# Kernel optimization log

Hardware: AMD Instinct MI355X
Metric: run time of the kernel (lower is better)

## Reference

```python
import jax, jax.numpy as jnp
import numpy as np

V, D, NH, DH, DFF, NL = 32000, 512, 8, 64, 2048, 6
S, B = 512, 8
NEG = -1e18


def layer_norm(x, g, b, eps=1e-5):
    m = x.mean(-1, keepdims=True)
    v = ((x - m) ** 2).mean(-1, keepdims=True)
    return (x - m) / jnp.sqrt(v + eps) * g + b


def mha(q, k, v, Wq, bq, Wk, bk, Wv, bv, Wo, bo, mask):
    Bq, Q, _ = q.shape
    K = k.shape[1]
    qh = (q @ Wq + bq).reshape(Bq, Q, NH, DH).transpose(0, 2, 1, 3)
    kh = (k @ Wk + bk).reshape(Bq, K, NH, DH).transpose(0, 2, 1, 3)
    vh = (v @ Wv + bv).reshape(Bq, K, NH, DH).transpose(0, 2, 1, 3)
    scores = jnp.einsum('bhqd,bhkd->bhqk', qh, kh) / np.sqrt(DH).astype(np.float32)
    scores = jnp.where(mask[:, None, :, :], NEG, scores)
    attn = jax.nn.softmax(scores, axis=-1)
    ctx = jnp.einsum('bhqk,bhkd->bhqd', attn, vh).transpose(0, 2, 1, 3).reshape(Bq, Q, NH * DH)
    return ctx @ Wo + bo


def positional_encoding(seq_len):
    pos = jnp.arange(seq_len, dtype=jnp.float32)[:, None]
    div = jnp.exp(jnp.arange(0, D, 2, dtype=jnp.float32) * (-np.log(10000.0) / D))
    pe = jnp.zeros((seq_len, D), jnp.float32)
    pe = pe.at[:, 0::2].set(jnp.sin(pos * div))
    pe = pe.at[:, 1::2].set(jnp.cos(pos * div))
    return pe


def setup_inputs() -> dict:
    key = jax.random.key(0)
    ks = iter(jax.random.split(key, 64))
    sc = 0.02
    pn = lambda shape: jax.random.normal(next(ks), shape, jnp.float32) * sc
    inp = {}
    inp['targets'] = jax.random.randint(next(ks), (S, B), 0, V)
    inp['memory'] = jax.random.normal(next(ks), (B, S, D), jnp.float32)
    inp['trg_mask'] = jnp.broadcast_to(jnp.triu(jnp.ones((S, S), bool), 1), (B, S, S))
    inp['memory_mask'] = jnp.zeros((B, S, S), bool)
    emb = pn((V, D)).at[1].set(0.0)  # padding_idx=1
    inp['emb'] = emb
    # stacked per-layer params
    for nm in ['Wq_s', 'Wk_s', 'Wv_s', 'Wo_s', 'Wq_c', 'Wk_c', 'Wv_c', 'Wo_c']:
        inp[nm] = pn((NL, D, D))
    for nm in ['bq_s', 'bk_s', 'bv_s', 'bo_s', 'bq_c', 'bk_c', 'bv_c', 'bo_c']:
        inp[nm] = jnp.zeros((NL, D), jnp.float32)
    inp['W1'] = pn((NL, D, DFF)); inp['b1'] = jnp.zeros((NL, DFF), jnp.float32)
    inp['W2'] = pn((NL, DFF, D)); inp['b2'] = jnp.zeros((NL, D), jnp.float32)
    for nm in ['g1', 'g2', 'g3']:
        inp[nm] = jnp.ones((NL, D), jnp.float32)
    for nm in ['be1', 'be2', 'be3']:
        inp[nm] = jnp.zeros((NL, D), jnp.float32)
    return inp


def reference(targets, memory, trg_mask, memory_mask, emb,
              Wq_s, bq_s, Wk_s, bk_s, Wv_s, bv_s, Wo_s, bo_s,
              Wq_c, bq_c, Wk_c, bk_c, Wv_c, bv_c, Wo_c, bo_c,
              W1, b1, W2, b2, g1, be1, g2, be2, g3, be3):
    # targets: (S, B) ints; embedding + sqrt(d) scale + sinusoidal PE
    x = emb[targets] * np.sqrt(D).astype(np.float32)      # (S, B, D)
    x = x + positional_encoding(targets.shape[0])[:, None, :]
    x = x.transpose(1, 0, 2)                              # (B, S, D)
    for i in range(NL):
        sa = mha(x, x, x, Wq_s[i], bq_s[i], Wk_s[i], bk_s[i], Wv_s[i], bv_s[i],
                 Wo_s[i], bo_s[i], trg_mask)
        x = layer_norm(x + sa, g1[i], be1[i])
        ca = mha(x, memory, memory, Wq_c[i], bq_c[i], Wk_c[i], bk_c[i], Wv_c[i], bv_c[i],
                 Wo_c[i], bo_c[i], memory_mask)
        x = layer_norm(x + ca, g2[i], be2[i])
        ff = jax.nn.relu(x @ W1[i] + b1[i]) @ W2[i] + b2[i]
        x = layer_norm(x + ff, g3[i], be3[i])
    return x
```

## Files before the change

### kernel.cpp

```cpp
#include <hip/hip_runtime.h>

typedef unsigned short u16;
typedef unsigned int   u32;
typedef __attribute__((ext_vector_type(4))) u16   u16x4;
typedef __attribute__((ext_vector_type(8))) u16   u16x8;
typedef __attribute__((ext_vector_type(8))) __bf16 bf16x8;
typedef __attribute__((ext_vector_type(4))) float f32x4;

#define DEV static __device__ __forceinline__

constexpr int DIM = 512, NHEAD = 8, DHEAD = 64, DFFN = 2048, NLAY = 6, SEQ = 512, BATCH = 8;
constexpr int MROWS = BATCH * SEQ;
constexpr long HD = (long)SEQ * DHEAD;
constexpr long SQ = (long)DIM * DIM;

DEV float bf2f(u16 u) { union { u32 i; float f; } x; x.i = (u32)u << 16; return x.f; }
DEV u16 f2bf(float f) { union { float f; u32 i; } x; x.f = f; u32 r = x.i + 0x7fffu + ((x.i >> 16) & 1u); return (u16)(r >> 16); }

DEV void gl_lds16(const u16* g, u16* l) {
    __builtin_amdgcn_global_load_lds((const __attribute__((address_space(1))) u32*)(const void*)g,
                                     (__attribute__((address_space(3))) u32*)(void*)l, 16, 0, 0);
}

struct TP { const float* in[8]; u16* out[8]; long ls[8]; };

__global__ __launch_bounds__(256) void transpose8(TP p)
{
    __shared__ u16 t[32][33];
    int z = blockIdx.z, which = z / NLAY, l = z % NLAY;
    const float* in = p.in[which] + (long)l * SQ;
    u16* out = p.out[which] + (long)l * p.ls[which];
    int k0 = blockIdx.y * 32, n0 = blockIdx.x * 32;
    int tx = threadIdx.x & 31, ty = threadIdx.x >> 5;
    #pragma unroll
    for (int i = ty; i < 32; i += 8) t[i][tx] = f2bf(in[(long)(k0 + i) * 512 + n0 + tx]);
    __syncthreads();
    #pragma unroll
    for (int i = ty; i < 32; i += 8) out[(long)(n0 + i) * 512 + k0 + tx] = t[tx][i];
}

__global__ __launch_bounds__(256) void transpose_w(const float* __restrict__ in, u16* __restrict__ out,
                                                   int K, int N, long outLS)
{
    __shared__ u16 t[32][33];
    long bi = (long)blockIdx.z * K * N, bo = (long)blockIdx.z * outLS;
    int k0 = blockIdx.y * 32, n0 = blockIdx.x * 32;
    int tx = threadIdx.x & 31, ty = threadIdx.x >> 5;
    #pragma unroll
    for (int i = ty; i < 32; i += 8) t[i][tx] = f2bf(in[bi + (long)(k0 + i) * N + n0 + tx]);
    __syncthreads();
    #pragma unroll
    for (int i = ty; i < 32; i += 8) out[bo + (long)(n0 + i) * K + k0 + tx] = t[tx][i];
}

__global__ __launch_bounds__(256) void concat_bias(const float* __restrict__ a, const float* __restrict__ b,
                                                   const float* __restrict__ c, float* __restrict__ out, int nsrc)
{
    int i = blockIdx.x * 256 + threadIdx.x;
    int col = i & 511, j = (i >> 9) % nsrc, l = i / (nsrc * 512);
    const float* s = (j == 0) ? a : (j == 1) ? b : c;
    out[i] = s[l * 512 + col];
}

__global__ __launch_bounds__(256) void conv_f32_bf16(const float* __restrict__ in, u16* __restrict__ out)
{
    long i = ((long)blockIdx.x * 256 + threadIdx.x) * 4;
    float4 v = *(const float4*)(in + i);
    u16x4 o; o.x = f2bf(v.x); o.y = f2bf(v.y); o.z = f2bf(v.z); o.w = f2bf(v.w);
    *(u16x4*)(out + i) = o;
}

__global__ __launch_bounds__(256) void embed_pe(const int* __restrict__ targets, const float* __restrict__ emb,
                                                float* __restrict__ x, u16* __restrict__ xb)
{
    int t4 = (blockIdx.x * 256 + threadIdx.x) * 4;
    int d = t4 & (DIM - 1);
    int s = (t4 >> 9) & (SEQ - 1);
    int b = t4 >> 18;
    int tok = targets[s * BATCH + b];
    float4 e = *(const float4*)(emb + (long)tok * DIM + d);
    float o[4]; u16x4 ob;
    const float ef[4] = { e.x, e.y, e.z, e.w };
    #pragma unroll
    for (int j = 0; j < 4; ++j) {
        int dd = d + j;
        float div = expf((float)(dd & ~1) * -0.017988946039016f);
        float ang = (float)s * div;
        float pe = (dd & 1) ? cosf(ang) : sinf(ang);
        float val = ef[j] * 22.627416997969522f + pe;
        o[j] = val; ob[j] = f2bf(val);
    }
    long idx = ((long)b * SEQ + s) * DIM + d;
    *(float4*)(x + idx) = *(const float4*)o;
    *(u16x4*)(xb + idx) = ob;
}

DEV void scat_sd(u16* dst, int mm, int col, float v) {
    dst[(long)((mm >> 9) * NHEAD + (col >> 6)) * HD + (long)(mm & 511) * DHEAD + (col & 63)] = f2bf(v);
}
DEV void scat_ds(u16* dst, int mm, int col, float v) {
    dst[(long)((mm >> 9) * NHEAD + (col >> 6)) * HD + (long)(col & 63) * SEQ + (mm & 511)] = f2bf(v);
}

template <int BN, int EPI>
__global__ __launch_bounds__(256) void gemm64(const u16* __restrict__ A0, const u16* __restrict__ A1,
                                              const u16* __restrict__ Bt,
                                              void* __restrict__ C0, void* __restrict__ C1, void* __restrict__ C2,
                                              const float* __restrict__ bias, int K, int ldc, int gx, int aSplit)
{
    constexpr int NCH = (64 + BN) / 8;
    constexpr int NI  = BN / 32;
    __shared__ __align__(16) u16 lds[2][NCH * 512];

    const int tid = threadIdx.x, lane = tid & 63, wid = tid >> 6;
    const int nwg = gridDim.x, bid = blockIdx.x;
    const int wg = (bid & 7) * (nwg >> 3) + (bid >> 3);
    const int m0 = (wg / gx) * 64, n0 = (wg % gx) * BN;
    const u16* A = (n0 < aSplit) ? A0 : A1;
    const int wr = (wid >> 1) * 32, wc = (wid & 1) * (BN / 2);
    const int fr = lane & 15, fq = lane >> 4;
    const int srow = lane >> 3;
    const int scol = ((lane & 7) ^ srow) * 8;

    f32x4 acc[2][NI] = {};

    auto stage = [&](int buf, int k0) {
        #pragma unroll
        for (int c = wid; c < 8; c += 4)
            gl_lds16(A + (long)(m0 + c * 8 + srow) * K + k0 + scol, &lds[buf][c * 512]);
        #pragma unroll
        for (int c = 8 + wid; c < NCH; c += 4)
            gl_lds16(Bt + (long)(n0 + (c - 8) * 8 + srow) * K + k0 + scol, &lds[buf][c * 512]);
    };

    const int nt = K >> 6;
    stage(0, 0);
    __syncthreads();
    int cur = 0;
    const int swz = (fr & 7) << 4;
    for (int t = 0; t < nt; ++t) {
        if (t + 1 < nt) stage(cur ^ 1, (t + 1) << 6);
        const char* lb = (const char*)&lds[cur][0];
        bf16x8 a[2][2], b[NI][2];
        #pragma unroll
        for (int mi = 0; mi < 2; ++mi)
            #pragma unroll
            for (int kk = 0; kk < 2; ++kk)
                a[mi][kk] = *(const bf16x8*)(lb + (wr + mi * 16 + fr) * 128 + ((kk * 64 + fq * 16) ^ swz));
        #pragma unroll
        for (int ni = 0; ni < NI; ++ni)
            #pragma unroll
            for (int kk = 0; kk < 2; ++kk)
                b[ni][kk] = *(const bf16x8*)(lb + (64 + wc + ni * 16 + fr) * 128 + ((kk * 64 + fq * 16) ^ swz));
        #pragma unroll
        for (int kk = 0; kk < 2; ++kk)
            #pragma unroll
            for (int mi = 0; mi < 2; ++mi)
                #pragma unroll
                for (int ni = 0; ni < NI; ++ni)
                    acc[mi][ni] = __builtin_amdgcn_mfma_f32_16x16x32_bf16(a[mi][kk], b[ni][kk], acc[mi][ni], 0, 0, 0);
        __syncthreads();
        cur ^= 1;
    }

    #pragma unroll
    for (int mi = 0; mi < 2; ++mi)
    #pragma unroll
    for (int ni = 0; ni < NI; ++ni)
    #pragma unroll
    for (int rr = 0; rr < 4; ++rr) {
        int mm = m0 + wr + mi * 16 + fq * 4 + rr;
        int nn = n0 + wc + ni * 16 + fr;
        float v = acc[mi][ni][rr] + bias[nn];
        if (EPI == 0) {
            ((u16*)C0)[(long)mm * ldc + nn] = f2bf(v);
        } else if (EPI == 1) {
            ((u16*)C0)[(long)mm * ldc + nn] = f2bf(fmaxf(v, 0.f));
        } else {
            int which = nn >> 9, col = nn & 511;
            if (which == 0)      scat_sd((u16*)C0, mm, col, v);
            else if (which == 1) scat_sd((u16*)C1, mm, col, v);
            else                 scat_ds((u16*)C2, mm, col, v);
        }
    }
}

template <bool CAUSAL>
__global__ __launch_bounds__(256) void flash_attn(const u16* __restrict__ qh, const u16* __restrict__ kh,
                                                  const u16* __restrict__ vT, u16* __restrict__ ctx)
{
    constexpr int KVB = 128;
    __shared__ __align__(16) u16 Kl[2][KVB * 64];
    __shared__ __align__(16) u16 Vl[2][64 * KVB];
    __shared__ __align__(16) u16 Pl[4][16 * KVB];
    const int lane = threadIdx.x & 63, wid = threadIdx.x >> 6;
    const int head = blockIdx.x >> 3, qt = blockIdx.x & 7;
    const int q0 = qt * 64;
    const long hb = (long)head * HD;
    const int fr = lane & 15, fq = lane >> 4;

    bf16x8 qf[2];
    #pragma unroll
    for (int kf = 0; kf < 2; ++kf)
        qf[kf] = *(const bf16x8*)(qh + hb + (long)(q0 + wid * 16 + fr) * 64 + kf * 32 + fq * 8);

    const int nt = CAUSAL ? (q0 >> 7) + 1 : SEQ / KVB;

    auto stage = [&](int buf, int t) {
        const long kv0 = (long)t * KVB;
        for (int c = wid; c < 16; c += 4)
            gl_lds16(kh + hb + (kv0 + c * 8 + (lane >> 3)) * 64 + (lane & 7) * 8, &Kl[buf][c * 512]);
        for (int c = wid; c < 16; c += 4)
            gl_lds16(vT + hb + (long)(c * 4 + (lane >> 4)) * SEQ + kv0 + (lane & 15) * 8, &Vl[buf][c * 512]);
    };

    float m[4], l[4];
    #pragma unroll
    for (int r = 0; r < 4; ++r) { m[r] = -3.0e38f; l[r] = 0.f; }
    f32x4 ao[4] = {};

    stage(0, 0);
    __syncthreads();
    int cur = 0;
    for (int t = 0; t < nt; ++t) {
        if (t + 1 < nt) stage(cur ^ 1, t + 1);
        f32x4 as[8] = {};
        #pragma unroll
        for (int nf = 0; nf < 8; ++nf)
            #pragma unroll
            for (int kf = 0; kf < 2; ++kf) {
                bf16x8 kfr = *(const bf16x8*)&Kl[cur][(nf * 16 + fr) * 64 + kf * 32 + fq * 8];
                as[nf] = __builtin_amdgcn_mfma_f32_16x16x32_bf16(qf[kf], kfr, as[nf], 0, 0, 0);
            }
        const int kv0 = t * KVB;
        const int qrow = q0 + wid * 16 + fq * 4;
        #pragma unroll
        for (int nf = 0; nf < 8; ++nf)
            #pragma unroll
            for (int rr = 0; rr < 4; ++rr) {
                float s = as[nf][rr] * 0.125f;
                if (CAUSAL && (kv0 + nf * 16 + fr > qrow + rr)) s = -3.0e38f;
                as[nf][rr] = s;
            }
        float p_scale[4];
        #pragma unroll
        for (int rr = 0; rr < 4; ++rr) {
            float mx = as[0][rr];
            #pragma unroll
            for (int nf = 1; nf < 8; ++nf) mx = fmaxf(mx, as[nf][rr]);
            #pragma unroll
            for (int o = 1; o < 16; o <<= 1) mx = fmaxf(mx, __shfl_xor(mx, o, 64));
            float mnew = fmaxf(m[rr], mx);
            p_scale[rr] = __expf(m[rr] - mnew);
            m[rr] = mnew;
        }
        float rsum[4] = {0.f, 0.f, 0.f, 0.f};
        u16* pw = &Pl[wid][0];
        #pragma unroll
        for (int nf = 0; nf < 8; ++nf)
            #pragma unroll
            for (int rr = 0; rr < 4; ++rr) {
                float p = __expf(as[nf][rr] - m[rr]);
                rsum[rr] += p;
                int row = fq * 4 + rr;
                int byte = (row * 256 + (nf * 16 + fr) * 2) ^ ((row & 7) << 4);
                *(u16*)((char*)pw + byte) = f2bf(p);
            }
        #pragma unroll
        for (int rr = 0; rr < 4; ++rr) {
            #pragma unroll
            for (int o = 1; o < 16; o <<= 1) rsum[rr] += __shfl_xor(rsum[rr], o, 64);
            l[rr] = l[rr] * p_scale[rr] + rsum[rr];
        }
        #pragma unroll
        for (int nf = 0; nf < 4; ++nf)
            #pragma unroll
            for (int rr = 0; rr < 4; ++rr) ao[nf][rr] *= p_scale[rr];
        #pragma unroll
        for (int kf = 0; kf < 4; ++kf) {
            int byte = (fr * 256 + kf * 64 + fq * 16) ^ ((fr & 7) << 4);
            bf16x8 pa = *(const bf16x8*)((const char*)pw + byte);
            #pragma unroll
            for (int nf = 0; nf < 4; ++nf) {
                bf16x8 vf = *(const bf16x8*)&Vl[cur][(nf * 16 + fr) * KVB + kf * 32 + fq * 8];
                ao[nf] = __builtin_amdgcn_mfma_f32_16x16x32_bf16(pa, vf, ao[nf], 0, 0, 0);
            }
        }
        __syncthreads();
        cur ^= 1;
    }
    const int b = head >> 3, h = head & 7;
    #pragma unroll
    for (int nf = 0; nf < 4; ++nf)
        #pragma unroll
        for (int rr = 0; rr < 4; ++rr) {
            int qq = q0 + wid * 16 + fq * 4 + rr;
            ctx[((long)(b * SEQ + qq)) * DIM + h * 64 + nf * 16 + fr] = f2bf(ao[nf][rr] / l[rr]);
        }
}

__global__ __launch_bounds__(256) void add_ln(const float* x, const u16* __restrict__ y,
                                              float* xo, u16* __restrict__ xb,
                                              const float* __restrict__ g, const float* __restrict__ be)
{
    int row = blockIdx.x * 4 + (threadIdx.x >> 6);
    int lane = threadIdx.x & 63;
    long off = (long)row * DIM + lane * 8;
    float v[8];
    {
        float4 a0 = *(const float4*)(x + off);
        float4 a1 = *(const float4*)(x + off + 4);
        u16x8 yv = *(const u16x8*)(y + off);
        v[0] = a0.x + bf2f(yv[0]); v[1] = a0.y + bf2f(yv[1]);
        v[2] = a0.z + bf2f(yv[2]); v[3] = a0.w + bf2f(yv[3]);
        v[4] = a1.x + bf2f(yv[4]); v[5] = a1.y + bf2f(yv[5]);
        v[6] = a1.z + bf2f(yv[6]); v[7] = a1.w + bf2f(yv[7]);
    }
    float sum = 0.f;
    #pragma unroll
    for (int j = 0; j < 8; ++j) sum += v[j];
    #pragma unroll
    for (int o = 32; o; o >>= 1) sum += __shfl_xor(sum, o, 64);
    float mean = sum * (1.0f / DIM);
    float vs = 0.f;
    #pragma unroll
    for (int j = 0; j < 8; ++j) { float d = v[j] - mean; vs += d * d; }
    #pragma unroll
    for (int o = 32; o; o >>= 1) vs += __shfl_xor(vs, o, 64);
    float rstd = rsqrtf(vs * (1.0f / DIM) + 1e-5f);
    float outv[8]; u16x8 ob;
    #pragma unroll
    for (int j = 0; j < 8; ++j) {
        int col = lane * 8 + j;
        float r = (v[j] - mean) * rstd * g[col] + be[col];
        outv[j] = r; ob[j] = f2bf(r);
    }
    *(float4*)(xo + off)     = *(const float4*)&outv[0];
    *(float4*)(xo + off + 4) = *(const float4*)&outv[4];
    *(u16x8*)(xb + off) = ob;
}

extern "C" void kernel_launch(void* const* d_in, const int* in_sizes, int n_in,
                              void* d_out, int out_size, void* d_ws, size_t ws_size,
                              hipStream_t stream)
{
    const int*   targets = (const int*)  d_in[0];
    const float* memory  = (const float*)d_in[1];
    const float* emb     = (const float*)d_in[4];
    const float* Wg[8]; for (int i = 0; i < 8; ++i) Wg[i] = (const float*)d_in[5 + i];
    const float* bg[8]; for (int i = 0; i < 8; ++i) bg[i] = (const float*)d_in[13 + i];
    const float* W1  = (const float*)d_in[21];
    const float* b1  = (const float*)d_in[22];
    const float* W2  = (const float*)d_in[23];
    const float* b2  = (const float*)d_in[24];
    const float* g1  = (const float*)d_in[25];
    const float* g2  = (const float*)d_in[26];
    const float* g3  = (const float*)d_in[27];
    const float* be1 = (const float*)d_in[28];
    const float* be2 = (const float*)d_in[29];
    const float* be3 = (const float*)d_in[30];

    char* w = (char*)d_ws;
    auto take = [&](size_t n) -> char* { char* p = w; w += (n + 255) & ~(size_t)255; return p; };
    u16*   wqkvT = (u16*)take((size_t)NLAY * 3 * SQ * 2);
    u16*   wcatT = (u16*)take((size_t)NLAY * 3 * SQ * 2);
    u16*   woT   = (u16*)take((size_t)NLAY * SQ * 2);
    u16*   wocT  = (u16*)take((size_t)NLAY * SQ * 2);
    u16*   w1T   = (u16*)take((size_t)NLAY * DIM * DFFN * 2);
    u16*   w2T   = (u16*)take((size_t)NLAY * DIM * DFFN * 2);
    float* bqkv  = (float*)take((size_t)NLAY * 3 * DIM * 4);
    float* bqkvc = (float*)take((size_t)NLAY * 3 * DIM * 4);
    float* x     = (float*)take((size_t)MROWS * DIM * 4);
    u16*   y     = (u16*)  take((size_t)MROWS * DIM * 2);
    u16*   xb    = (u16*)  take((size_t)MROWS * DIM * 2);
    u16*   memb  = (u16*)  take((size_t)MROWS * DIM * 2);
    u16*   qh    = (u16*)  take((size_t)MROWS * DIM * 2);
    u16*   kh    = (u16*)  take((size_t)MROWS * DIM * 2);
    u16*   vT    = (u16*)  take((size_t)MROWS * DIM * 2);
    u16*   ctx   = (u16*)  take((size_t)MROWS * DIM * 2);
    u16*   h1    = (u16*)  take((size_t)MROWS * DFFN * 2);

    TP tp;
    tp.in[0] = Wg[0]; tp.out[0] = wqkvT;          tp.ls[0] = 3 * SQ;
    tp.in[1] = Wg[1]; tp.out[1] = wqkvT + SQ;     tp.ls[1] = 3 * SQ;
    tp.in[2] = Wg[2]; tp.out[2] = wqkvT + 2 * SQ; tp.ls[2] = 3 * SQ;
    tp.in[3] = Wg[3]; tp.out[3] = woT;            tp.ls[3] = SQ;
    tp.in[4] = Wg[4]; tp.out[4] = wcatT;          tp.ls[4] = 3 * SQ;
    tp.in[5] = Wg[5]; tp.out[5] = wcatT + SQ;     tp.ls[5] = 3 * SQ;
    tp.in[6] = Wg[6]; tp.out[6] = wcatT + 2 * SQ; tp.ls[6] = 3 * SQ;
    tp.in[7] = Wg[7]; tp.out[7] = wocT;           tp.ls[7] = SQ;
    transpose8<<<dim3(16, 16, 8 * NLAY), 256, 0, stream>>>(tp);
    transpose_w<<<dim3(64, 16, NLAY), 256, 0, stream>>>(W1, w1T, DIM, DFFN, (long)DIM * DFFN);
    transpose_w<<<dim3(16, 64, NLAY), 256, 0, stream>>>(W2, w2T, DFFN, DIM, (long)DIM * DFFN);
    concat_bias<<<NLAY * 3 * DIM / 256, 256, 0, stream>>>(bg[0], bg[1], bg[2], bqkv, 3);
    concat_bias<<<NLAY * 3 * DIM / 256, 256, 0, stream>>>(bg[4], bg[5], bg[6], bqkvc, 3);
    conv_f32_bf16<<<2048, 256, 0, stream>>>(memory, memb);
    embed_pe<<<2048, 256, 0, stream>>>(targets, emb, x, xb);

    const int BIG = 1 << 30;
    for (int i = 0; i < NLAY; ++i) {
        const u16 *wqkv = wqkvT + (long)i * 3 * SQ, *wcat = wcatT + (long)i * 3 * SQ;
        const u16 *wo = woT + (long)i * SQ, *woc = wocT + (long)i * SQ;
        const u16 *w1t = w1T + (long)i * DIM * DFFN, *w2t = w2T + (long)i * DIM * DFFN;
        const float *bo = bg[3] + i * DIM, *boc = bg[7] + i * DIM;

        gemm64<128, 4><<<768, 256, 0, stream>>>(xb, xb, wqkv, qh, kh, vT, bqkv + i * 3 * DIM, DIM, 0, 12, BIG);
        flash_attn<true><<<BATCH * NHEAD * (SEQ / 64), 256, 0, stream>>>(qh, kh, vT, ctx);
        gemm64<64, 0><<<512, 256, 0, stream>>>(ctx, ctx, wo, y, nullptr, nullptr, bo, DIM, DIM, 8, BIG);
        add_ln<<<MROWS / 4, 256, 0, stream>>>(x, y, x, xb, g1 + i * DIM, be1 + i * DIM);

        gemm64<128, 4><<<768, 256, 0, stream>>>(xb, memb, wcat, qh, kh, vT, bqkvc + i * 3 * DIM, DIM, 0, 12, 512);
        flash_attn<false><<<BATCH * NHEAD * (SEQ / 64), 256, 0, stream>>>(qh, kh, vT, ctx);
        gemm64<64, 0><<<512, 256, 0, stream>>>(ctx, ctx, woc, y, nullptr, nullptr, boc, DIM, DIM, 8, BIG);
        add_ln<<<MROWS / 4, 256, 0, stream>>>(x, y, x, xb, g2 + i * DIM, be2 + i * DIM);

        gemm64<128, 1><<<1024, 256, 0, stream>>>(xb, xb, w1t, h1, nullptr, nullptr, b1 + i * DFFN, DIM, DFFN, 16, BIG);
        gemm64<64, 0><<<512, 256, 0, stream>>>(h1, h1, w2t, y, nullptr, nullptr, b2 + i * DIM, DFFN, DIM, 8, BIG);
        float* xo = (i == NLAY - 1) ? (float*)d_out : x;
        add_ln<<<MROWS / 4, 256, 0, stream>>>(x, y, xo, xb, g3 + i * DIM, be3 + i * DIM);
    }
}
```

Before: 978.8 us.

## Use 128x128 GEMM tiles for QKV/FFN1 and swizzle flash-attn K/V LDS

```diff
diff --git a/kernel.cpp b/kernel.cpp
--- a/kernel.cpp
+++ b/kernel.cpp
@@ -102,35 +102,36 @@
     dst[(long)((mm >> 9) * NHEAD + (col >> 6)) * HD + (long)(col & 63) * SEQ + (mm & 511)] = f2bf(v);
 }
 
-template <int BN, int EPI>
-__global__ __launch_bounds__(256) void gemm64(const u16* __restrict__ A0, const u16* __restrict__ A1,
+template <int BM, int BN, int EPI>
+__global__ __launch_bounds__(256) void gemm_t(const u16* __restrict__ A0, const u16* __restrict__ A1,
                                               const u16* __restrict__ Bt,
                                               void* __restrict__ C0, void* __restrict__ C1, void* __restrict__ C2,
                                               const float* __restrict__ bias, int K, int ldc, int gx, int aSplit)
 {
-    constexpr int NCH = (64 + BN) / 8;
-    constexpr int NI  = BN / 32;
+    constexpr int NCHA = BM / 8;
+    constexpr int NCH  = (BM + BN) / 8;
+    constexpr int MI   = BM / 32;
+    constexpr int NI   = BN / 32;
     __shared__ __align__(16) u16 lds[2][NCH * 512];
 
     const int tid = threadIdx.x, lane = tid & 63, wid = tid >> 6;
     const int nwg = gridDim.x, bid = blockIdx.x;
     const int wg = (bid & 7) * (nwg >> 3) + (bid >> 3);
-    const int m0 = (wg / gx) * 64, n0 = (wg % gx) * BN;
+    const int m0 = (wg / gx) * BM, n0 = (wg % gx) * BN;
     const u16* A = (n0 < aSplit) ? A0 : A1;
-    const int wr = (wid >> 1) * 32, wc = (wid & 1) * (BN / 2);
+    const int wr = (wid >> 1) * (BM / 2), wc = (wid & 1) * (BN / 2);
     const int fr = lane & 15, fq = lane >> 4;
     const int srow = lane >> 3;
     const int scol = ((lane & 7) ^ srow) * 8;
 
-    f32x4 acc[2][NI] = {};
+    f32x4 acc[MI][NI] = {};
 
     auto stage = [&](int buf, int k0) {
         #pragma unroll
-        for (int c = wid; c < 8; c += 4)
-            gl_lds16(A + (long)(m0 + c * 8 + srow) * K + k0 + scol, &lds[buf][c * 512]);
-        #pragma unroll
-        for (int c = 8 + wid; c < NCH; c += 4)
-            gl_lds16(Bt + (long)(n0 + (c - 8) * 8 + srow) * K + k0 + scol, &lds[buf][c * 512]);
+        for (int c = wid; c < NCH; c += 4) {
+            if (c < NCHA) gl_lds16(A  + (long)(m0 + c * 8 + srow) * K + k0 + scol, &lds[buf][c * 512]);
+            else          gl_lds16(Bt + (long)(n0 + (c - NCHA) * 8 + srow) * K + k0 + scol, &lds[buf][c * 512]);
+        }
     };
 
     const int nt = K >> 6;
@@ -141,9 +142,9 @@
     for (int t = 0; t < nt; ++t) {
         if (t + 1 < nt) stage(cur ^ 1, (t + 1) << 6);
         const char* lb = (const char*)&lds[cur][0];
-        bf16x8 a[2][2], b[NI][2];
-        #pragma unroll
-        for (int mi = 0; mi < 2; ++mi)
+        bf16x8 a[MI][2], b[NI][2];
+        #pragma unroll
+        for (int mi = 0; mi < MI; ++mi)
             #pragma unroll
             for (int kk = 0; kk < 2; ++kk)
                 a[mi][kk] = *(const bf16x8*)(lb + (wr + mi * 16 + fr) * 128 + ((kk * 64 + fq * 16) ^ swz));
@@ -151,11 +152,11 @@
         for (int ni = 0; ni < NI; ++ni)
             #pragma unroll
             for (int kk = 0; kk < 2; ++kk)
-                b[ni][kk] = *(const bf16x8*)(lb + (64 + wc + ni * 16 + fr) * 128 + ((kk * 64 + fq * 16) ^ swz));
+                b[ni][kk] = *(const bf16x8*)(lb + (BM + wc + ni * 16 + fr) * 128 + ((kk * 64 + fq * 16) ^ swz));
         #pragma unroll
         for (int kk = 0; kk < 2; ++kk)
             #pragma unroll
-            for (int mi = 0; mi < 2; ++mi)
+            for (int mi = 0; mi < MI; ++mi)
                 #pragma unroll
                 for (int ni = 0; ni < NI; ++ni)
                     acc[mi][ni] = __builtin_amdgcn_mfma_f32_16x16x32_bf16(a[mi][kk], b[ni][kk], acc[mi][ni], 0, 0, 0);
@@ -164,7 +165,7 @@
     }
 
     #pragma unroll
-    for (int mi = 0; mi < 2; ++mi)
+    for (int mi = 0; mi < MI; ++mi)
     #pragma unroll
     for (int ni = 0; ni < NI; ++ni)
     #pragma unroll
@@ -198,6 +199,7 @@
     const int q0 = qt * 64;
     const long hb = (long)head * HD;
     const int fr = lane & 15, fq = lane >> 4;
+    const int swz = (fr & 7) << 4;
 
     bf16x8 qf[2];
     #pragma unroll
@@ -208,10 +210,16 @@
 
     auto stage = [&](int buf, int t) {
         const long kv0 = (long)t * KVB;
+        const int kr = lane >> 3;
+        const int kcol = ((lane & 7) ^ kr) * 8;
         for (int c = wid; c < 16; c += 4)
-            gl_lds16(kh + hb + (kv0 + c * 8 + (lane >> 3)) * 64 + (lane & 7) * 8, &Kl[buf][c * 512]);
-        for (int c = wid; c < 16; c += 4)
-            gl_lds16(vT + hb + (long)(c * 4 + (lane >> 4)) * SEQ + kv0 + (lane & 15) * 8, &Vl[buf][c * 512]);
+            gl_lds16(kh + hb + (kv0 + c * 8 + kr) * 64 + kcol, &Kl[buf][c * 512]);
+        const int vr = lane >> 4;
+        for (int c = wid; c < 16; c += 4) {
+            int row = c * 4 + vr;
+            int vcol = ((lane & 15) ^ (row & 7)) * 8;
+            gl_lds16(vT + hb + (long)row * SEQ + kv0 + vcol, &Vl[buf][c * 512]);
+        }
     };
 
     float m[4], l[4];
@@ -225,13 +233,16 @@
     for (int t = 0; t < nt; ++t) {
         if (t + 1 < nt) stage(cur ^ 1, t + 1);
         f32x4 as[8] = {};
+        const char* kb = (const char*)&Kl[cur][0];
+        __builtin_amdgcn_s_setprio(1);
         #pragma unroll
         for (int nf = 0; nf < 8; ++nf)
             #pragma unroll
             for (int kf = 0; kf < 2; ++kf) {
-                bf16x8 kfr = *(const bf16x8*)&Kl[cur][(nf * 16 + fr) * 64 + kf * 32 + fq * 8];
+                bf16x8 kfr = *(const bf16x8*)(kb + (nf * 16 + fr) * 128 + ((kf * 64 + fq * 16) ^ swz));
                 as[nf] = __builtin_amdgcn_mfma_f32_16x16x32_bf16(qf[kf], kfr, as[nf], 0, 0, 0);
             }
+        __builtin_amdgcn_s_setprio(0);
         const int kv0 = t * KVB;
         const int qrow = q0 + wid * 16 + fq * 4;
         #pragma unroll
@@ -276,16 +287,19 @@
         for (int nf = 0; nf < 4; ++nf)
             #pragma unroll
             for (int rr = 0; rr < 4; ++rr) ao[nf][rr] *= p_scale[rr];
+        const char* vb = (const char*)&Vl[cur][0];
+        __builtin_amdgcn_s_setprio(1);
         #pragma unroll
         for (int kf = 0; kf < 4; ++kf) {
-            int byte = (fr * 256 + kf * 64 + fq * 16) ^ ((fr & 7) << 4);
-            bf16x8 pa = *(const bf16x8*)((const char*)pw + byte);
+            int pbyte = (fr * 256 + kf * 64 + fq * 16) ^ swz;
+            bf16x8 pa = *(const bf16x8*)((const char*)pw + pbyte);
             #pragma unroll
             for (int nf = 0; nf < 4; ++nf) {
-                bf16x8 vf = *(const bf16x8*)&Vl[cur][(nf * 16 + fr) * KVB + kf * 32 + fq * 8];
+                bf16x8 vf = *(const bf16x8*)(vb + (nf * 16 + fr) * 256 + ((kf * 64 + fq * 16) ^ swz));
                 ao[nf] = __builtin_amdgcn_mfma_f32_16x16x32_bf16(pa, vf, ao[nf], 0, 0, 0);
             }
         }
+        __builtin_amdgcn_s_setprio(0);
         __syncthreads();
         cur ^= 1;
     }
@@ -404,18 +418,18 @@
         const u16 *w1t = w1T + (long)i * DIM * DFFN, *w2t = w2T + (long)i * DIM * DFFN;
         const float *bo = bg[3] + i * DIM, *boc = bg[7] + i * DIM;
 
-        gemm64<128, 4><<<768, 256, 0, stream>>>(xb, xb, wqkv, qh, kh, vT, bqkv + i * 3 * DIM, DIM, 0, 12, BIG);
+        gemm_t<128, 128, 4><<<384, 256, 0, stream>>>(xb, xb, wqkv, qh, kh, vT, bqkv + i * 3 * DIM, DIM, 0, 12, BIG);
         flash_attn<true><<<BATCH * NHEAD * (SEQ / 64), 256, 0, stream>>>(qh, kh, vT, ctx);
-        gemm64<64, 0><<<512, 256, 0, stream>>>(ctx, ctx, wo, y, nullptr, nullptr, bo, DIM, DIM, 8, BIG);
+        gemm_t<64, 64, 0><<<512, 256, 0, stream>>>(ctx, ctx, wo, y, nullptr, nullptr, bo, DIM, DIM, 8, BIG);
         add_ln<<<MROWS / 4, 256, 0, stream>>>(x, y, x, xb, g1 + i * DIM, be1 + i * DIM);
 
-        gemm64<128, 4><<<768, 256, 0, stream>>>(xb, memb, wcat, qh, kh, vT, bqkvc + i * 3 * DIM, DIM, 0, 12, 512);
+        gemm_t<128, 128, 4><<<384, 256, 0, stream>>>(xb, memb, wcat, qh, kh, vT, bqkvc + i * 3 * DIM, DIM, 0, 12, 512);
         flash_attn<false><<<BATCH * NHEAD * (SEQ / 64), 256, 0, stream>>>(qh, kh, vT, ctx);
-        gemm64<64, 0><<<512, 256, 0, stream>>>(ctx, ctx, woc, y, nullptr, nullptr, boc, DIM, DIM, 8, BIG);
+        gemm_t<64, 64, 0><<<512, 256, 0, stream>>>(ctx, ctx, woc, y, nullptr, nullptr, boc, DIM, DIM, 8, BIG);
         add_ln<<<MROWS / 4, 256, 0, stream>>>(x, y, x, xb, g2 + i * DIM, be2 + i * DIM);
 
-        gemm64<128, 1><<<1024, 256, 0, stream>>>(xb, xb, w1t, h1, nullptr, nullptr, b1 + i * DFFN, DIM, DFFN, 16, BIG);
-        gemm64<64, 0><<<512, 256, 0, stream>>>(h1, h1, w2t, y, nullptr, nullptr, b2 + i * DIM, DFFN, DIM, 8, BIG);
+        gemm_t<128, 128, 1><<<512, 256, 0, stream>>>(xb, xb, w1t, h1, nullptr, nullptr, b1 + i * DFFN, DIM, DFFN, 16, BIG);
+        gemm_t<64, 64, 0><<<512, 256, 0, stream>>>(h1, h1, w2t, y, nullptr, nullptr, b2 + i * DIM, DFFN, DIM, 8, BIG);
         float* xo = (i == NLAY - 1) ? (float*)d_out : x;
         add_ln<<<MROWS / 4, 256, 0, stream>>>(x, y, xo, xb, g3 + i * DIM, be3 + i * DIM);
     }
```

Result: faster. 925.0 us (-5.5%).
